# Kernel tuning notes

Hardware: AMD Instinct MI355X
Metric: run time of the kernel (lower is better)

Reference implementation:

```python
import jax, jax.numpy as jnp
from jax import lax
import numpy as np

B, TW, TC = 128, 256, 25   # sentences, words per sentence, chars per word
V, D, H = 128, 32, 64      # char vocab, char embed dim, lstm units


def setup_inputs() -> dict:
    key = jax.random.key(0)
    k0, k1, k2, k3 = jax.random.split(key, 4)
    chars = jax.random.randint(k0, (B, TW, TC), 0, V)
    E = jax.random.normal(k1, (V, D), dtype=jnp.float32) * 0.05
    W = jax.random.normal(k2, (D, 4 * H), dtype=jnp.float32) * (1.0 / np.sqrt(D))
    U = jax.random.normal(k3, (H, 4 * H), dtype=jnp.float32) * (1.0 / np.sqrt(H))
    b = jnp.zeros((4 * H,), dtype=jnp.float32)
    return {"chars": chars, "E": E, "W": W, "U": U, "b": b}


def _char_lstm(chars, E, W, U, b):
    Bq, Tw, Tc = chars.shape
    d = E.shape[1]
    h_units = U.shape[0]
    N = Bq * Tw  # independent per-word sequences
    x = E[chars].reshape(N, Tc, d)                       # [N, Tc, D]
    # precompute input projection for all timesteps (one big GEMM)
    xz = jnp.einsum('ntd,dk->ntk', x, W) + b             # [N, Tc, 4H]
    z_seq = jnp.moveaxis(xz, 1, 0)                       # [Tc, N, 4H]

    def step(carry, z_t):
        h, c = carry
        z = z_t + h @ U                                  # [N, 4H]
        i, f, g, o = jnp.split(z, 4, axis=-1)            # Keras gate order i,f,c,o
        i = jax.nn.sigmoid(i)
        f = jax.nn.sigmoid(f)
        g = jnp.tanh(g)
        o = jax.nn.sigmoid(o)
        c = f * c + i * g
        h = o * jnp.tanh(c)
        return (h, c), None

    h0 = jnp.zeros((N, h_units), dtype=x.dtype)
    c0 = jnp.zeros((N, h_units), dtype=x.dtype)
    (h_last, _), _ = lax.scan(step, (h0, c0), z_seq)
    return h_last.reshape(Bq, Tw, h_units)               # return_sequences=False


def reference(chars, E, W, U, b):
    return _char_lstm(chars, E, W, U, b)
```

## Files before the change

### kernel.cpp

```cpp
#include <hip/hip_runtime.h>
#include <hip/hip_bf16.h>


#define SEQ_M 16
#define TC_LEN 25
#define H_N 64
#define D_N 32
#define G4_N 256
#define V_N 128

typedef __attribute__((ext_vector_type(8))) short bf16x8;
typedef __attribute__((ext_vector_type(4))) float f32x4;
typedef __attribute__((ext_vector_type(2))) float f32x2;
typedef __attribute__((ext_vector_type(4))) int i32x4;

#define SCALE_SIG (-1.4426950408889634f)
#define SCALE_G   ( 2.8853900817779268f)

__device__ __forceinline__ ushort bf16_rne(float x) {
    const uint u = __float_as_uint(x);
    return (ushort)((u + 0x7fffu + ((u >> 16) & 1u)) >> 16);
}
__device__ __forceinline__ float bf16_tof(ushort h) {
    return __uint_as_float(((uint)h) << 16);
}
__device__ __forceinline__ int hswz(int row, int kbyte) {
    const int b = row * 128 + kbyte;
    return b ^ ((row & 7) << 4);
}

__global__ void ew_precompute(const float* __restrict__ E,
                              const float* __restrict__ W,
                              const float* __restrict__ b,
                              float* __restrict__ EWr) {
    const int v = blockIdx.x;
    const int j = threadIdx.x;
    float acc = b[j];
#pragma unroll
    for (int d = 0; d < D_N; ++d)
        acc = fmaf(E[v * D_N + d], W[d * G4_N + j], acc);
    const int tile = j >> 6, c16 = j & 63;
    const float scale = (tile == 2) ? SCALE_G : SCALE_SIG;
    EWr[v * G4_N + c16 * 4 + tile] = acc * scale;
}

__global__ void u_pack(const float* __restrict__ U, ushort* __restrict__ Upk) {
    const int k   = blockIdx.x;
    const int col = threadIdx.x;
    const float scale = ((col >> 6) == 2) ? SCALE_G : SCALE_SIG;
    const float uv = U[k * G4_N + col] * scale;
    Upk[col * 64 + k] = bf16_rne(uv);
}

__global__ __launch_bounds__(256, 4) void char_lstm_mfma(
    const int* __restrict__ chars,
    const ushort* __restrict__ Upk,
    const float* __restrict__ EWr,
    float* __restrict__ out)
{
    const int j = threadIdx.x;
    const int w = j >> 6;
    const int l = j & 63;
    const int q = l >> 4;
    const int n16 = l & 15;
    const int c16 = w * 16 + n16;
    const int seq0 = blockIdx.x * SEQ_M;

    __shared__ int ibuf[TC_LEN][SEQ_M];
    __shared__ ushort hbuf[2][SEQ_M * H_N];

    for (int idx = j; idx < TC_LEN * SEQ_M; idx += 256) {
        const int s = idx & 15, tt = idx >> 4;
        ibuf[tt][s] = chars[(seq0 + s) * TC_LEN + tt] << 10;
    }

    bf16x8 bh[4][2];
#pragma unroll
    for (int tile = 0; tile < 4; ++tile) {
        const ushort* ub = Upk + (tile * 64 + c16) * 64 + 8 * q;
#pragma unroll
        for (int ks = 0; ks < 2; ++ks)
            bh[tile][ks] = *(const bf16x8*)(ub + ks * 32);
    }

    __syncthreads();

    const int offA0 = hswz(n16, 16 * q);
    const int offA1 = hswz(n16, 64 + 16 * q);
    int offW[4];
#pragma unroll
    for (int r = 0; r < 4; ++r) offW[r] = hswz(4 * q + r, c16 * 2);
    const char* ewbase = (const char*)EWr;
    const uint  c16b   = (uint)(c16 * 16);

    f32x2 cP[2] = {{0.0f, 0.0f}, {0.0f, 0.0f}};
    f32x4 ewv[4];
    f32x4 acc[4];
    const f32x4 zero4 = {0.0f, 0.0f, 0.0f, 0.0f};

#define ACT_BODY(HN, ADD_EW, WRITE_OUT)                                       \
    {                                                                         \
        _Pragma("unroll")                                                     \
        for (int p = 0; p < 2; ++p) {                                         \
            const int r0 = 2 * p, r1 = 2 * p + 1;                             \
            f32x2 z0, z1, z2, z3;                                             \
            if (ADD_EW) {                                                     \
                z0[0] = acc[0][r0] + ewv[r0][0]; z0[1] = acc[0][r1] + ewv[r1][0]; \
                z1[0] = acc[1][r0] + ewv[r0][1]; z1[1] = acc[1][r1] + ewv[r1][1]; \
                z2[0] = acc[2][r0] + ewv[r0][2]; z2[1] = acc[2][r1] + ewv[r1][2]; \
                z3[0] = acc[3][r0] + ewv[r0][3]; z3[1] = acc[3][r1] + ewv[r1][3]; \
            } else {                                                          \
                z0[0] = ewv[r0][0]; z0[1] = ewv[r1][0];                       \
                z1[0] = ewv[r0][1]; z1[1] = ewv[r1][1];                       \
                z2[0] = ewv[r0][2]; z2[1] = ewv[r1][2];                       \
                z3[0] = ewv[r0][3]; z3[1] = ewv[r1][3];                       \
            }                                                                 \
            f32x2 A, B, C, D;                                                 \
            A[0] = __builtin_amdgcn_exp2f(z0[0]); A[1] = __builtin_amdgcn_exp2f(z0[1]); \
            B[0] = __builtin_amdgcn_exp2f(z1[0]); B[1] = __builtin_amdgcn_exp2f(z1[1]); \
            C[0] = __builtin_amdgcn_exp2f(z2[0]); C[1] = __builtin_amdgcn_exp2f(z2[1]); \
            D[0] = __builtin_amdgcn_exp2f(z3[0]); D[1] = __builtin_amdgcn_exp2f(z3[1]); \
            const f32x2 di = A + 1.0f, df = B + 1.0f, dg = C + 1.0f;          \
            const f32x2 m1 = di * dg;                                         \
            const f32x2 num = cP[p] * m1 + (C - 1.0f) * df;                   \
            const f32x2 qa = m1 * df;                                         \
            f32x2 Q;                                                          \
            Q[0] = __builtin_amdgcn_rcpf(qa[0]);                              \
            Q[1] = __builtin_amdgcn_rcpf(qa[1]);                              \
            cP[p] = num * Q;                                                  \
            const f32x2 cs = cP[p] * SCALE_G;                                 \
            f32x2 E2;                                                         \
            E2[0] = __builtin_amdgcn_exp2f(cs[0]);                            \
            E2[1] = __builtin_amdgcn_exp2f(cs[1]);                            \
            const f32x2 nh = E2 - 1.0f;                                       \
            const f32x2 Ph = (D + 1.0f) * (E2 + 1.0f);                        \
            f32x2 R;                                                          \
            R[0] = __builtin_amdgcn_rcpf(Ph[0]);                              \
            R[1] = __builtin_amdgcn_rcpf(Ph[1]);                              \
            const f32x2 h = nh * R;                                           \
            _Pragma("unroll")                                                 \
            for (int e = 0; e < 2; ++e) {                                     \
                const int r = 2 * p + e;                                      \
                if (WRITE_OUT) {                                              \
                    out[(seq0 + 4 * q + r) * H_N + c16] = h[e];               \
                } else {                                                      \
                    *(ushort*)((HN) + offW[r]) = bf16_rne(h[e]);              \
                }                                                             \
            }                                                                 \
        }                                                                     \
    }

#define PREFETCH_EW(T1)                                                       \
    {                                                                         \
        const i32x4 cv = *(const i32x4*)&ibuf[(T1)][4 * q];                   \
        _Pragma("unroll")                                                     \
        for (int r = 0; r < 4; ++r)                                           \
            ewv[r] = *(const f32x4*)(ewbase + (uint)(cv[r]) + c16b);          \
    }

#define MFMA_CLUSTER(RB)                                                      \
    {                                                                         \
        const bf16x8 ah0 = *(const bf16x8*)((RB) + offA0);                    \
        const bf16x8 ah1 = *(const bf16x8*)((RB) + offA1);                    \
        __builtin_amdgcn_s_setprio(1);                                        \
        _Pragma("unroll")                                                     \
        for (int tile = 0; tile < 4; ++tile)                                  \
            acc[tile] = __builtin_amdgcn_mfma_f32_16x16x32_bf16(              \
                ah0, bh[tile][0], zero4, 0, 0, 0);                            \
        _Pragma("unroll")                                                     \
        for (int tile = 0; tile < 4; ++tile)                                  \
            acc[tile] = __builtin_amdgcn_mfma_f32_16x16x32_bf16(              \
                ah1, bh[tile][1], acc[tile], 0, 0, 0);                        \
        __builtin_amdgcn_s_setprio(0);                                        \
    }

    char* b0 = (char*)&hbuf[0][0];
    char* b1 = (char*)&hbuf[1][0];

    PREFETCH_EW(0);
    ACT_BODY(b0, 0, 0);
    PREFETCH_EW(1);
    __syncthreads();

    for (int tp = 0; tp < 11; ++tp) {
        MFMA_CLUSTER(b0);
        ACT_BODY(b1, 1, 0);
        PREFETCH_EW(2 * tp + 2);
        __syncthreads();
        MFMA_CLUSTER(b1);
        ACT_BODY(b0, 1, 0);
        PREFETCH_EW(2 * tp + 3);
        __syncthreads();
    }

    MFMA_CLUSTER(b0);
    ACT_BODY(b1, 1, 0);
    PREFETCH_EW(24);
    __syncthreads();

    MFMA_CLUSTER(b1);
    ACT_BODY(b1, 1, 1);

#undef ACT_BODY
#undef PREFETCH_EW
#undef MFMA_CLUSTER
}

extern "C" void kernel_launch(void* const* d_in, const int* in_sizes, int n_in,
                              void* d_out, int out_size, void* d_ws, size_t ws_size,
                              hipStream_t stream) {
    const int*   chars = (const int*)d_in[0];
    const float* E     = (const float*)d_in[1];
    const float* W     = (const float*)d_in[2];
    const float* U     = (const float*)d_in[3];
    const float* b     = (const float*)d_in[4];
    float* out = (float*)d_out;
    float*  EWr = (float*)d_ws;
    ushort* Upk = (ushort*)((char*)d_ws + 131072);

    const int N = in_sizes[0] / TC_LEN;
    const int blocks = N / SEQ_M;

    ew_precompute<<<V_N, G4_N, 0, stream>>>(E, W, b, EWr);
    u_pack<<<H_N, G4_N, 0, stream>>>(U, Upk);
    char_lstm_mfma<<<blocks, 256, 0, stream>>>(chars, Upk, EWr, out);
}
```

Measured before the change: 72.33 us.

## Run each 16-sequence LSTM tile in a single wave without barriers

The four-wave block is replaced by one 64-thread wave per 16 sequences. That wave computes all four 16-unit hidden groups itself, so it holds the full packed U in registers and software-pipelines the EW loads, MFMAs and activations across the groups. Because the whole hidden state is produced and consumed by one wave, the per-timestep __syncthreads and the double-buffered h in LDS are no longer needed. In exchange, each wave does four times the serial work and the kernel launches a quarter as many waves. Register pressure is higher (about 128 VGPRs just for U fragments), which can limit latency hiding.

```diff
diff --git a/kernel.cpp b/kernel.cpp
--- a/kernel.cpp
+++ b/kernel.cpp
@@ -2,7 +2,6 @@
 #include <hip/hip_bf16.h>
 
 
-#define SEQ_M 16
 #define TC_LEN 25
 #define H_N 64
 #define D_N 32
@@ -52,68 +51,97 @@
     Upk[col * 64 + k] = bf16_rne(uv);
 }
 
-__global__ __launch_bounds__(256, 4) void char_lstm_mfma(
+__global__ __launch_bounds__(64, 2) void char_lstm_wave(
     const int* __restrict__ chars,
     const ushort* __restrict__ Upk,
     const float* __restrict__ EWr,
     float* __restrict__ out)
 {
-    const int j = threadIdx.x;
-    const int w = j >> 6;
-    const int l = j & 63;
+    const int l = threadIdx.x;
     const int q = l >> 4;
     const int n16 = l & 15;
-    const int c16 = w * 16 + n16;
-    const int seq0 = blockIdx.x * SEQ_M;
-
-    __shared__ int ibuf[TC_LEN][SEQ_M];
-    __shared__ ushort hbuf[2][SEQ_M * H_N];
-
-    for (int idx = j; idx < TC_LEN * SEQ_M; idx += 256) {
+    const int seq0 = blockIdx.x * 16;
+
+    __shared__ int ibuf[TC_LEN][16];
+    __shared__ ushort hbuf[16 * H_N];
+
+    for (int idx = l; idx < TC_LEN * 16; idx += 64) {
         const int s = idx & 15, tt = idx >> 4;
         ibuf[tt][s] = chars[(seq0 + s) * TC_LEN + tt] << 10;
     }
 
-    bf16x8 bh[4][2];
-#pragma unroll
-    for (int tile = 0; tile < 4; ++tile) {
-        const ushort* ub = Upk + (tile * 64 + c16) * 64 + 8 * q;
-#pragma unroll
-        for (int ks = 0; ks < 2; ++ks)
-            bh[tile][ks] = *(const bf16x8*)(ub + ks * 32);
-    }
-
-    __syncthreads();
+    bf16x8 bh[4][4][2];
+#pragma unroll
+    for (int ug = 0; ug < 4; ++ug)
+#pragma unroll
+        for (int g = 0; g < 4; ++g) {
+            const ushort* ub = Upk + (g * 64 + ug * 16 + n16) * 64 + 8 * q;
+            bh[ug][g][0] = *(const bf16x8*)(ub);
+            bh[ug][g][1] = *(const bf16x8*)(ub + 32);
+        }
 
     const int offA0 = hswz(n16, 16 * q);
     const int offA1 = hswz(n16, 64 + 16 * q);
-    int offW[4];
-#pragma unroll
-    for (int r = 0; r < 4; ++r) offW[r] = hswz(4 * q + r, c16 * 2);
+    int rowb[4], rswz[4];
+#pragma unroll
+    for (int r = 0; r < 4; ++r) {
+        rowb[r] = (4 * q + r) * 128;
+        rswz[r] = ((4 * q + r) & 7) << 4;
+    }
+    const int  colw   = n16 * 2;
+    const uint colb0  = (uint)(n16 * 16);
     const char* ewbase = (const char*)EWr;
-    const uint  c16b   = (uint)(c16 * 16);
-
-    f32x2 cP[2] = {{0.0f, 0.0f}, {0.0f, 0.0f}};
-    f32x4 ewv[4];
+    char* hb = (char*)hbuf;
+    float* outb = out + (seq0 + 4 * q) * H_N + n16;
+
+    f32x2 cP[4][2];
+#pragma unroll
+    for (int ug = 0; ug < 4; ++ug) {
+        cP[ug][0] = (f32x2){0.0f, 0.0f};
+        cP[ug][1] = (f32x2){0.0f, 0.0f};
+    }
     f32x4 acc[4];
+    f32x4 ewv[2][4];
     const f32x4 zero4 = {0.0f, 0.0f, 0.0f, 0.0f};
 
-#define ACT_BODY(HN, ADD_EW, WRITE_OUT)                                       \
+#define EW_LOAD(PP, UG)                                                       \
+    {                                                                         \
+        _Pragma("unroll")                                                     \
+        for (int r = 0; r < 4; ++r)                                           \
+            ewv[PP][r] = *(const f32x4*)(ewbase + (uint)cv[r] + colb0 +       \
+                                         (UG) * 256u);                        \
+    }
+
+#define MFMA_G(UG)                                                            \
+    {                                                                         \
+        __builtin_amdgcn_s_setprio(1);                                        \
+        _Pragma("unroll")                                                     \
+        for (int g = 0; g < 4; ++g)                                           \
+            acc[g] = __builtin_amdgcn_mfma_f32_16x16x32_bf16(                 \
+                ah0, bh[UG][g][0], zero4, 0, 0, 0);                           \
+        _Pragma("unroll")                                                     \
+        for (int g = 0; g < 4; ++g)                                           \
+            acc[g] = __builtin_amdgcn_mfma_f32_16x16x32_bf16(                 \
+                ah1, bh[UG][g][1], acc[g], 0, 0, 0);                          \
+        __builtin_amdgcn_s_setprio(0);                                        \
+    }
+
+#define ACT_G(UG, PP, ADD_EW, WRITE_OUT)                                      \
     {                                                                         \
         _Pragma("unroll")                                                     \
         for (int p = 0; p < 2; ++p) {                                         \
             const int r0 = 2 * p, r1 = 2 * p + 1;                             \
             f32x2 z0, z1, z2, z3;                                             \
             if (ADD_EW) {                                                     \
-                z0[0] = acc[0][r0] + ewv[r0][0]; z0[1] = acc[0][r1] + ewv[r1][0]; \
-                z1[0] = acc[1][r0] + ewv[r0][1]; z1[1] = acc[1][r1] + ewv[r1][1]; \
-                z2[0] = acc[2][r0] + ewv[r0][2]; z2[1] = acc[2][r1] + ewv[r1][2]; \
-                z3[0] = acc[3][r0] + ewv[r0][3]; z3[1] = acc[3][r1] + ewv[r1][3]; \
+                z0[0] = acc[0][r0] + ewv[PP][r0][0]; z0[1] = acc[0][r1] + ewv[PP][r1][0]; \
+                z1[0] = acc[1][r0] + ewv[PP][r0][1]; z1[1] = acc[1][r1] + ewv[PP][r1][1]; \
+                z2[0] = acc[2][r0] + ewv[PP][r0][2]; z2[1] = acc[2][r1] + ewv[PP][r1][2]; \
+                z3[0] = acc[3][r0] + ewv[PP][r0][3]; z3[1] = acc[3][r1] + ewv[PP][r1][3]; \
             } else {                                                          \
-                z0[0] = ewv[r0][0]; z0[1] = ewv[r1][0];                       \
-                z1[0] = ewv[r0][1]; z1[1] = ewv[r1][1];                       \
-                z2[0] = ewv[r0][2]; z2[1] = ewv[r1][2];                       \
-                z3[0] = ewv[r0][3]; z3[1] = ewv[r1][3];                       \
+                z0[0] = ewv[PP][r0][0]; z0[1] = ewv[PP][r1][0];               \
+                z1[0] = ewv[PP][r0][1]; z1[1] = ewv[PP][r1][1];               \
+                z2[0] = ewv[PP][r0][2]; z2[1] = ewv[PP][r1][2];               \
+                z3[0] = ewv[PP][r0][3]; z3[1] = ewv[PP][r1][3];               \
             }                                                                 \
             f32x2 A, B, C, D;                                                 \
             A[0] = __builtin_amdgcn_exp2f(z0[0]); A[1] = __builtin_amdgcn_exp2f(z0[1]); \
@@ -122,13 +150,13 @@
             D[0] = __builtin_amdgcn_exp2f(z3[0]); D[1] = __builtin_amdgcn_exp2f(z3[1]); \
             const f32x2 di = A + 1.0f, df = B + 1.0f, dg = C + 1.0f;          \
             const f32x2 m1 = di * dg;                                         \
-            const f32x2 num = cP[p] * m1 + (C - 1.0f) * df;                   \
+            const f32x2 num = cP[UG][p] * m1 + (C - 1.0f) * df;               \
             const f32x2 qa = m1 * df;                                         \
             f32x2 Q;                                                          \
             Q[0] = __builtin_amdgcn_rcpf(qa[0]);                              \
             Q[1] = __builtin_amdgcn_rcpf(qa[1]);                              \
-            cP[p] = num * Q;                                                  \
-            const f32x2 cs = cP[p] * SCALE_G;                                 \
+            cP[UG][p] = num * Q;                                              \
+            const f32x2 cs = cP[UG][p] * SCALE_G;                             \
             f32x2 E2;                                                         \
             E2[0] = __builtin_amdgcn_exp2f(cs[0]);                            \
             E2[1] = __builtin_amdgcn_exp2f(cs[1]);                            \
@@ -142,68 +170,57 @@
             for (int e = 0; e < 2; ++e) {                                     \
                 const int r = 2 * p + e;                                      \
                 if (WRITE_OUT) {                                              \
-                    out[(seq0 + 4 * q + r) * H_N + c16] = h[e];               \
+                    outb[r * H_N + (UG) * 16] = h[e];                         \
                 } else {                                                      \
-                    *(ushort*)((HN) + offW[r]) = bf16_rne(h[e]);              \
+                    *(ushort*)(hb + rowb[r] +                                 \
+                               (((UG) * 32 + colw) ^ rswz[r])) =              \
+                        bf16_rne(h[e]);                                       \
                 }                                                             \
             }                                                                 \
         }                                                                     \
     }
 
-#define PREFETCH_EW(T1)                                                       \
-    {                                                                         \
-        const i32x4 cv = *(const i32x4*)&ibuf[(T1)][4 * q];                   \
-        _Pragma("unroll")                                                     \
-        for (int r = 0; r < 4; ++r)                                           \
-            ewv[r] = *(const f32x4*)(ewbase + (uint)(cv[r]) + c16b);          \
-    }
-
-#define MFMA_CLUSTER(RB)                                                      \
-    {                                                                         \
-        const bf16x8 ah0 = *(const bf16x8*)((RB) + offA0);                    \
-        const bf16x8 ah1 = *(const bf16x8*)((RB) + offA1);                    \
-        __builtin_amdgcn_s_setprio(1);                                        \
-        _Pragma("unroll")                                                     \
-        for (int tile = 0; tile < 4; ++tile)                                  \
-            acc[tile] = __builtin_amdgcn_mfma_f32_16x16x32_bf16(              \
-                ah0, bh[tile][0], zero4, 0, 0, 0);                            \
-        _Pragma("unroll")                                                     \
-        for (int tile = 0; tile < 4; ++tile)                                  \
-            acc[tile] = __builtin_amdgcn_mfma_f32_16x16x32_bf16(              \
-                ah1, bh[tile][1], acc[tile], 0, 0, 0);                        \
-        __builtin_amdgcn_s_setprio(0);                                        \
-    }
-
-    char* b0 = (char*)&hbuf[0][0];
-    char* b1 = (char*)&hbuf[1][0];
-
-    PREFETCH_EW(0);
-    ACT_BODY(b0, 0, 0);
-    PREFETCH_EW(1);
-    __syncthreads();
-
-    for (int tp = 0; tp < 11; ++tp) {
-        MFMA_CLUSTER(b0);
-        ACT_BODY(b1, 1, 0);
-        PREFETCH_EW(2 * tp + 2);
-        __syncthreads();
-        MFMA_CLUSTER(b1);
-        ACT_BODY(b0, 1, 0);
-        PREFETCH_EW(2 * tp + 3);
-        __syncthreads();
-    }
-
-    MFMA_CLUSTER(b0);
-    ACT_BODY(b1, 1, 0);
-    PREFETCH_EW(24);
-    __syncthreads();
-
-    MFMA_CLUSTER(b1);
-    ACT_BODY(b1, 1, 1);
-
-#undef ACT_BODY
-#undef PREFETCH_EW
-#undef MFMA_CLUSTER
+#define TS_BODY(T, WO)                                                        \
+    {                                                                         \
+        const i32x4 cv = *(const i32x4*)&ibuf[(T)][4 * q];                    \
+        const bf16x8 ah0 = *(const bf16x8*)(hb + offA0);                      \
+        const bf16x8 ah1 = *(const bf16x8*)(hb + offA1);                      \
+        EW_LOAD(0, 0);                                                        \
+        MFMA_G(0);                                                            \
+        EW_LOAD(1, 1);                                                        \
+        ACT_G(0, 0, 1, WO);                                                   \
+        MFMA_G(1);                                                            \
+        EW_LOAD(0, 2);                                                        \
+        ACT_G(1, 1, 1, WO);                                                   \
+        MFMA_G(2);                                                            \
+        EW_LOAD(1, 3);                                                        \
+        ACT_G(2, 0, 1, WO);                                                   \
+        MFMA_G(3);                                                            \
+        ACT_G(3, 1, 1, WO);                                                   \
+    }
+
+    {
+        const i32x4 cv = *(const i32x4*)&ibuf[0][4 * q];
+        EW_LOAD(0, 0);
+        EW_LOAD(1, 1);
+        ACT_G(0, 0, 0, 0);
+        EW_LOAD(0, 2);
+        ACT_G(1, 1, 0, 0);
+        EW_LOAD(1, 3);
+        ACT_G(2, 0, 0, 0);
+        ACT_G(3, 1, 0, 0);
+    }
+
+    for (int t = 1; t < 24; ++t) {
+        TS_BODY(t, 0);
+    }
+
+    TS_BODY(24, 1);
+
+#undef EW_LOAD
+#undef MFMA_G
+#undef ACT_G
+#undef TS_BODY
 }
 
 extern "C" void kernel_launch(void* const* d_in, const int* in_sizes, int n_in,
@@ -219,9 +236,9 @@
     ushort* Upk = (ushort*)((char*)d_ws + 131072);
 
     const int N = in_sizes[0] / TC_LEN;
-    const int blocks = N / SEQ_M;
+    const int blocks = N / 16;
 
     ew_precompute<<<V_N, G4_N, 0, stream>>>(E, W, b, EWr);
     u_pack<<<H_N, G4_N, 0, stream>>>(U, Upk);
-    char_lstm_mfma<<<blocks, 256, 0, stream>>>(chars, Upk, EWr, out);
-}
+    char_lstm_wave<<<blocks, 64, 0, stream>>>(chars, Upk, EWr, out);
+}
```

New measurement: 74.90 us. +3.6%, slower.
